# Optimization experiments

Hardware: AMD Instinct MI355X
Metric: run time of the kernel (lower is better)

## Reference

```python
import jax, jax.numpy as jnp
from jax import lax
import numpy as np

DEPTH, D_MODEL, D_INNER, D_STATE, DT_RANK = 24, 192, 384, 16, 12
EPS = 1e-5

def _layernorm(x, w, b):
    m = x.mean(-1, keepdims=True)
    v = ((x - m) ** 2).mean(-1, keepdims=True)
    return (x - m) * lax.rsqrt(v + EPS) * w + b

def _silu(x):
    return x * jax.nn.sigmoid(x)

def _mamba_mixer(x, in_w, cw, cb, xp_w, dtw, dtb, a_log, dvec, out_w):
    # x: (B, L, D_MODEL)
    B, L, _ = x.shape
    xz = jnp.einsum('bld,ed->ble', x, in_w)            # (B, L, 2*D_INNER)
    xi, z = xz[..., :D_INNER], xz[..., D_INNER:]
    # causal depthwise conv1d, kernel 4 (left-pad 3, truncate to L)
    xt = jnp.moveaxis(xi, 1, 2)                        # (B, D_INNER, L)
    xt = jnp.pad(xt, ((0, 0), (0, 0), (3, 0)))
    xt = lax.conv_general_dilated(xt, cw[:, None, :], (1,), 'VALID',
                                  dimension_numbers=('NCH', 'OIH', 'NCH'),
                                  feature_group_count=D_INNER)
    xt = _silu(xt + cb[None, :, None])
    xc = jnp.moveaxis(xt, 1, 2)                        # (B, L, D_INNER)
    x_dbl = jnp.einsum('bld,ed->ble', xc, xp_w)        # (B, L, DT_RANK+2*D_STATE)
    dt = x_dbl[..., :DT_RANK]
    Bm = x_dbl[..., DT_RANK:DT_RANK + D_STATE]         # (B, L, N)
    Cm = x_dbl[..., DT_RANK + D_STATE:]                # (B, L, N)
    delta = jax.nn.softplus(jnp.einsum('blr,dr->bld', dt, dtw) + dtb)  # (B, L, D_INNER)
    A = -jnp.exp(a_log)                                # (D_INNER, N)
    dA = jnp.exp(delta[..., None] * A)                 # (B, L, D_INNER, N)
    dBx = (delta * xc)[..., None] * Bm[:, :, None, :]  # (B, L, D_INNER, N)

    def step(h, inp):
        dA_t, dBx_t, C_t = inp
        h = dA_t * h + dBx_t
        y = jnp.einsum('bdn,bn->bd', h, C_t)
        return h, y

    h0 = jnp.zeros((B, D_INNER, D_STATE), x.dtype)
    _, ys = lax.scan(step, h0, (jnp.moveaxis(dA, 1, 0), jnp.moveaxis(dBx, 1, 0), jnp.moveaxis(Cm, 1, 0)))
    y = jnp.moveaxis(ys, 0, 1) + xc * dvec             # (B, L, D_INNER)
    y = y * _silu(z)
    return jnp.einsum('ble,de->bld', y, out_w)

def _forward(x, patch_w, patch_b, norm_w, norm_b, in_proj_w, conv_w, conv_b,
             x_proj_w, dt_w, dt_b, A_log, Dp, out_proj_w, normf_w, normf_b, head_w, head_b):
    # patch embed: conv 16x16 stride 16 -> (B, 192, 14, 14) -> (B, 196, 192)
    h = lax.conv_general_dilated(x, patch_w, (16, 16), 'VALID',
                                 dimension_numbers=('NCHW', 'OIHW', 'NCHW'))
    h = h + patch_b[None, :, None, None]
    B = h.shape[0]
    hidden = h.reshape(B, D_MODEL, -1).transpose(0, 2, 1)  # (B, L, D)
    residual = None
    for d in range(DEPTH):
        residual = hidden if residual is None else residual + hidden
        normed = _layernorm(residual, norm_w[d], norm_b[d])
        hidden = _mamba_mixer(normed, in_proj_w[d], conv_w[d], conv_b[d], x_proj_w[d],
                              dt_w[d], dt_b[d], A_log[d], Dp[d], out_proj_w[d])
    residual = residual + hidden
    feat = _layernorm(residual, normf_w, normf_b)
    pooled = feat.mean(axis=1)                           # final_pool_type='mean'
    return pooled @ head_w.T + head_b                    # (B, num_classes)

def setup_inputs() -> dict:
    key = jax.random.key(0)
    ks = jax.random.split(key, 16)
    s = 0.05
    return {
        'x': jax.random.normal(ks[0], (64, 3, 224, 224), jnp.float32),
        'patch_w': jax.random.normal(ks[1], (192, 3, 16, 16), jnp.float32) * s,
        'patch_b': jnp.zeros((192,), jnp.float32),
        'norm_w': jnp.ones((DEPTH, D_MODEL), jnp.float32),
        'norm_b': jnp.zeros((DEPTH, D_MODEL), jnp.float32),
        'in_proj_w': jax.random.normal(ks[2], (DEPTH, 2 * D_INNER, D_MODEL), jnp.float32) * s,
        'conv_w': jax.random.normal(ks[3], (DEPTH, D_INNER, 4), jnp.float32) * 0.3,
        'conv_b': jnp.zeros((DEPTH, D_INNER), jnp.float32),
        'x_proj_w': jax.random.normal(ks[4], (DEPTH, DT_RANK + 2 * D_STATE, D_INNER), jnp.float32) * s,
        'dt_w': jax.random.normal(ks[5], (DEPTH, D_INNER, DT_RANK), jnp.float32) * s,
        'dt_b': jax.random.uniform(ks[6], (DEPTH, D_INNER), jnp.float32, -4.0, -2.0),
        'A_log': jnp.log(jnp.broadcast_to(jnp.arange(1, D_STATE + 1, dtype=jnp.float32), (DEPTH, D_INNER, D_STATE))),
        'Dp': jnp.ones((DEPTH, D_INNER), jnp.float32),
        'out_proj_w': jax.random.normal(ks[7], (DEPTH, D_MODEL, D_INNER), jnp.float32) * s,
        'normf_w': jnp.ones((D_MODEL,), jnp.float32),
        'normf_b': jnp.zeros((D_MODEL,), jnp.float32),
        'head_w': jax.random.normal(ks[8], (1000, D_MODEL), jnp.float32) * s,
        'head_b': jnp.zeros((1000,), jnp.float32),
    }

def reference(x, patch_w, patch_b, norm_w, norm_b, in_proj_w, conv_w, conv_b,
              x_proj_w, dt_w, dt_b, A_log, Dp, out_proj_w, normf_w, normf_b, head_w, head_b):
    return _forward(x, patch_w, patch_b, norm_w, norm_b, in_proj_w, conv_w, conv_b,
                    x_proj_w, dt_w, dt_b, A_log, Dp, out_proj_w, normf_w, normf_b, head_w, head_b)
```

## Files before the change

kernel.cpp:

```cpp
#include <hip/hip_runtime.h>
#include <math.h>


#define DEPTH 24
#define DM 192
#define DI 384
#define DS 16
#define DR 12
#define SEQL 196
#define BATCH 64
#define MROWS (BATCH*SEQL)
#define XDP 8624
#define LOG2E 1.44269504088896340736f

typedef unsigned short ushort_t;
typedef __bf16 bf16x8 __attribute__((ext_vector_type(8)));
typedef float f32x4 __attribute__((ext_vector_type(4)));

__device__ __forceinline__ float sigmoidf_(float x) { return 1.f / (1.f + __expf(-x)); }

__device__ __forceinline__ ushort_t f2bf(float f) {
    union { float f; unsigned u; } c; c.f = f;
    unsigned u = c.u;
    return (ushort_t)((u + 0x7FFFu + ((u >> 16) & 1u)) >> 16);
}
__device__ __forceinline__ float bf2f(ushort_t u) {
    union { unsigned u; float f; } c; c.u = ((unsigned)u) << 16;
    return c.f;
}

__device__ __forceinline__ void load_lds16(const ushort_t* g, ushort_t* l) {
    __builtin_amdgcn_global_load_lds((__attribute__((address_space(1))) void*)g,
                                     (__attribute__((address_space(3))) void*)l, 16, 0, 0);
}

template<int CTRL>
__device__ __forceinline__ float dpp_mov(float oldv, float src) {
    return __builtin_bit_cast(float, __builtin_amdgcn_update_dpp(
        __builtin_bit_cast(int, oldv), __builtin_bit_cast(int, src),
        CTRL, 0xF, 0xF, false));
}

__device__ __forceinline__ float row16_sum(float v) {
    v += dpp_mov<0xB1>(0.f, v);
    v += dpp_mov<0x4E>(0.f, v);
    v += dpp_mov<0x141>(0.f, v);
    v += dpp_mov<0x140>(0.f, v);
    return v;
}

__global__ void f2bf4_kernel(const float* __restrict__ src, ushort_t* __restrict__ dst, int n4) {
    int i = blockIdx.x * 256 + threadIdx.x;
    if (i >= n4) return;
    float4 v = ((const float4*)src)[i];
    union { ushort_t s[4]; uint2 u; } o;
    o.s[0] = f2bf(v.x); o.s[1] = f2bf(v.y); o.s[2] = f2bf(v.z); o.s[3] = f2bf(v.w);
    ((uint2*)dst)[i] = o.u;
}

__global__ void xp_pad_kernel(const float* __restrict__ src, ushort_t* __restrict__ dst) {
    int i = blockIdx.x * 256 + threadIdx.x;
    if (i >= DEPTH * 64 * 384) return;
    int col = i % 384, row = (i / 384) & 63, d = i / (384 * 64);
    float v = (row < 44) ? src[(size_t)d * 44 * 384 + row * 384 + col] : 0.f;
    dst[i] = f2bf(v);
}

template<bool BF>
__global__ void ln_kernel(float* __restrict__ residual, const float* __restrict__ hidden,
                          const float* __restrict__ w, const float* __restrict__ b,
                          void* __restrict__ out_) {
    int wave = threadIdx.x >> 6, lane = threadIdx.x & 63;
    int row = blockIdx.x * 4 + wave;
    float* rr = residual + (size_t)row * DM;
    const float* hr = hidden + (size_t)row * DM;
    float v0 = rr[lane]       + hr[lane];
    float v1 = rr[lane + 64]  + hr[lane + 64];
    float v2 = rr[lane + 128] + hr[lane + 128];
    rr[lane] = v0; rr[lane + 64] = v1; rr[lane + 128] = v2;
    float s = v0 + v1 + v2;
    #pragma unroll
    for (int off = 32; off > 0; off >>= 1) s += __shfl_down(s, off);
    float mean = __shfl(s, 0) * (1.f / DM);
    float d0 = v0 - mean, d1 = v1 - mean, d2 = v2 - mean;
    float q = d0 * d0 + d1 * d1 + d2 * d2;
    #pragma unroll
    for (int off = 32; off > 0; off >>= 1) q += __shfl_down(q, off);
    float rstd = rsqrtf(__shfl(q, 0) * (1.f / DM) + 1e-5f);
    float o0 = d0 * rstd * w[lane]       + b[lane];
    float o1 = d1 * rstd * w[lane + 64]  + b[lane + 64];
    float o2 = d2 * rstd * w[lane + 128] + b[lane + 128];
    if constexpr (BF) {
        ushort_t* o = (ushort_t*)out_ + (size_t)row * DM;
        o[lane] = f2bf(o0); o[lane + 64] = f2bf(o1); o[lane + 128] = f2bf(o2);
    } else {
        float* o = (float*)out_ + (size_t)row * DM;
        o[lane] = o0; o[lane + 64] = o1; o[lane + 128] = o2;
    }
}

template<int BN, int WM, int WN, int NST, bool TC>
__global__ __launch_bounds__(256, 2) void gemm_mfma(const ushort_t* __restrict__ A,
        const ushort_t* __restrict__ W, float* __restrict__ C, int K, int ldC) {
    constexpr int FM = 128 / (WM * 16);
    constexpr int FN = BN / (WN * 16);
    __shared__ ushort_t sA[128 * 32];
    __shared__ ushort_t sB[BN * 32];
    const int t = threadIdx.x;
    const int wave = t >> 6, lane = t & 63;
    const int lr = lane & 15, lq = lane >> 4;
    const int wr = wave / WN, wc = wave % WN;
    const int m0 = blockIdx.x * 128, n0 = blockIdx.y * BN;
    const int wbase = t & ~63;

    f32x4 acc[FM][FN];
    #pragma unroll
    for (int i = 0; i < FM; i++)
        #pragma unroll
        for (int j = 0; j < FN; j++) acc[i][j] = f32x4{0.f, 0.f, 0.f, 0.f};

    for (int k0 = 0; k0 < K; k0 += 32) {
        __syncthreads();
        #pragma unroll
        for (int c = 0; c < 2; c++) {
            int s = c * 256 + t;
            int row = s >> 2;
            int quad = (s & 3) ^ ((row >> 1) & 3);
            load_lds16(A + (size_t)(m0 + row) * K + k0 + quad * 8,
                       sA + (size_t)(c * 256 + wbase) * 8);
        }
        #pragma unroll
        for (int c = 0; c < BN * 4 / 256; c++) {
            int s = c * 256 + t;
            int row = s >> 2;
            int quad = (s & 3) ^ ((row >> 1) & 3);
            load_lds16(W + (size_t)(n0 + row) * K + k0 + quad * 8,
                       sB + (size_t)(c * 256 + wbase) * 8);
        }
        __syncthreads();
        bf16x8 af[FM], bfr[FN];
        #pragma unroll
        for (int i = 0; i < FM; i++) {
            int row = wr * FM * 16 + i * 16 + lr;
            int slot = (row << 2) | (lq ^ ((row >> 1) & 3));
            af[i] = *(const bf16x8*)&sA[(size_t)slot * 8];
        }
        #pragma unroll
        for (int j = 0; j < FN; j++) {
            int row = wc * FN * 16 + j * 16 + lr;
            int slot = (row << 2) | (lq ^ ((row >> 1) & 3));
            bfr[j] = *(const bf16x8*)&sB[(size_t)slot * 8];
        }
        #pragma unroll
        for (int i = 0; i < FM; i++)
            #pragma unroll
            for (int j = 0; j < FN; j++)
                acc[i][j] = __builtin_amdgcn_mfma_f32_16x16x32_bf16(af[i], bfr[j], acc[i][j], 0, 0, 0);
    }
    int crow0 = m0 + wr * FM * 16 + lq * 4;
    int ccol0 = n0 + wc * FN * 16 + lr;
    if constexpr (TC) {
        #pragma unroll
        for (int i = 0; i < FM; i++) {
            int m = crow0 + i * 16;
            int bb = m / 196, l = m % 196;
            #pragma unroll
            for (int j = 0; j < FN; j++) {
                int col = ccol0 + j * 16;
                if (col < 44) {
                    float4 v = {acc[i][j][0], acc[i][j][1], acc[i][j][2], acc[i][j][3]};
                    *(float4*)(C + (size_t)bb * XDP + (size_t)col * 196 + l) = v;
                }
            }
        }
    } else {
        #pragma unroll
        for (int i = 0; i < FM; i++)
            #pragma unroll
            for (int j = 0; j < FN; j++) {
                if (wc * FN + j >= NST) continue;
                float* cp = C + (size_t)(crow0 + i * 16) * ldC + ccol0 + j * 16;
                #pragma unroll
                for (int r = 0; r < 4; r++) cp[(size_t)r * ldC] = acc[i][j][r];
            }
    }
}

__global__ __launch_bounds__(256, 2) void gemm_patch_mfma(const ushort_t* __restrict__ Xbf,
        const ushort_t* __restrict__ Wbf, const float* __restrict__ bias, float* __restrict__ C) {
    constexpr int FM = 2, FN = 4;
    __shared__ ushort_t sA[128 * 32];
    __shared__ ushort_t sB[64 * 32];
    const int t = threadIdx.x;
    const int wave = t >> 6, lane = t & 63;
    const int lr = lane & 15, lq = lane >> 4;
    const int m0 = blockIdx.x * 128, n0 = blockIdx.y * 64;
    const int wbase = t & ~63;

    const ushort_t* abase[2];
    int aquad[2];
    #pragma unroll
    for (int c = 0; c < 2; c++) {
        int s = c * 256 + t;
        int row = s >> 2;
        aquad[c] = (s & 3) ^ ((row >> 1) & 3);
        int m = m0 + row;
        int b = m / 196, r = m % 196, py = r / 14, px = r % 14;
        abase[c] = Xbf + (size_t)b * 150528 + py * 3584 + px * 16;
    }
    int brow = t >> 2;
    int bquad = (t & 3) ^ ((brow >> 1) & 3);
    const ushort_t* bbase = Wbf + (size_t)(n0 + brow) * 768 + bquad * 8;

    f32x4 acc[FM][FN];
    #pragma unroll
    for (int i = 0; i < FM; i++)
        #pragma unroll
        for (int j = 0; j < FN; j++) acc[i][j] = f32x4{0.f, 0.f, 0.f, 0.f};

    for (int k0 = 0; k0 < 768; k0 += 32) {
        __syncthreads();
        #pragma unroll
        for (int c = 0; c < 2; c++) {
            int k = k0 + aquad[c] * 8;
            int ci = k >> 8, ky = (k >> 4) & 15, kx0 = k & 15;
            load_lds16(abase[c] + ci * 50176 + ky * 224 + kx0,
                       sA + (size_t)(c * 256 + wbase) * 8);
        }
        load_lds16(bbase + k0, sB + (size_t)wbase * 8);
        __syncthreads();
        bf16x8 af[FM], bfr[FN];
        #pragma unroll
        for (int i = 0; i < FM; i++) {
            int row = wave * FM * 16 + i * 16 + lr;
            int slot = (row << 2) | (lq ^ ((row >> 1) & 3));
            af[i] = *(const bf16x8*)&sA[(size_t)slot * 8];
        }
        #pragma unroll
        for (int j = 0; j < FN; j++) {
            int row = j * 16 + lr;
            int slot = (row << 2) | (lq ^ ((row >> 1) & 3));
            bfr[j] = *(const bf16x8*)&sB[(size_t)slot * 8];
        }
        #pragma unroll
        for (int i = 0; i < FM; i++)
            #pragma unroll
            for (int j = 0; j < FN; j++)
                acc[i][j] = __builtin_amdgcn_mfma_f32_16x16x32_bf16(af[i], bfr[j], acc[i][j], 0, 0, 0);
    }
    int crow0 = m0 + wave * FM * 16 + lq * 4;
    int ccol0 = n0 + lr;
    #pragma unroll
    for (int i = 0; i < FM; i++)
        #pragma unroll
        for (int j = 0; j < FN; j++) {
            int col = ccol0 + j * 16;
            float bv = bias[col];
            float* cp = C + (size_t)(crow0 + i * 16) * DM + col;
            #pragma unroll
            for (int r = 0; r < 4; r++) cp[(size_t)r * DM] = acc[i][j][r] + bv;
        }
}

template<bool BIAS>
__global__ __launch_bounds__(256, 2) void gemm64(const float* __restrict__ A,
        const float* __restrict__ W, const float* __restrict__ bias,
        float* __restrict__ C, int M, int N, int K) {
    __shared__ float As[32][68];
    __shared__ float Ws[32][68];
    int t = threadIdx.x;
    int m0 = blockIdx.x * 64, n0 = blockIdx.y * 64;
    int lr = t >> 2, lk = (t & 3) * 4;
    int am = m0 + lr; bool avld = am < M;
    const float* Ap = A + (size_t)(avld ? am : 0) * K + lk;
    int wn = n0 + lr; bool wv = wn < N;
    const float* Wp = W + (size_t)(wv ? wn : 0) * K + lk;
    int tm = (t >> 4) * 4, tn = (t & 15) * 4;
    float acc[4][4];
    #pragma unroll
    for (int i = 0; i < 4; i++)
        #pragma unroll
        for (int j = 0; j < 4; j++) acc[i][j] = 0.f;

    for (int k0 = 0; k0 < K; k0 += 32) {
        float4 a0 = make_float4(0.f, 0.f, 0.f, 0.f), a1 = a0, w0 = a0, w1 = a0;
        if (avld) { a0 = *(const float4*)(Ap + k0); a1 = *(const float4*)(Ap + k0 + 16); }
        if (wv)   { w0 = *(const float4*)(Wp + k0); w1 = *(const float4*)(Wp + k0 + 16); }
        __syncthreads();
        As[lk + 0][lr] = a0.x; As[lk + 1][lr] = a0.y; As[lk + 2][lr] = a0.z; As[lk + 3][lr] = a0.w;
        As[lk + 16][lr] = a1.x; As[lk + 17][lr] = a1.y; As[lk + 18][lr] = a1.z; As[lk + 19][lr] = a1.w;
        Ws[lk + 0][lr] = w0.x; Ws[lk + 1][lr] = w0.y; Ws[lk + 2][lr] = w0.z; Ws[lk + 3][lr] = w0.w;
        Ws[lk + 16][lr] = w1.x; Ws[lk + 17][lr] = w1.y; Ws[lk + 18][lr] = w1.z; Ws[lk + 19][lr] = w1.w;
        __syncthreads();
        #pragma unroll
        for (int kk = 0; kk < 32; kk++) {
            float4 x0 = *(const float4*)&As[kk][tm];
            float4 y0 = *(const float4*)&Ws[kk][tn];
            float av[4] = {x0.x, x0.y, x0.z, x0.w};
            float bv[4] = {y0.x, y0.y, y0.z, y0.w};
            #pragma unroll
            for (int i = 0; i < 4; i++)
                #pragma unroll
                for (int j = 0; j < 4; j++) acc[i][j] = fmaf(av[i], bv[j], acc[i][j]);
        }
    }
    #pragma unroll
    for (int i = 0; i < 4; i++) {
        int m = m0 + tm + i;
        if (m >= M) continue;
        float* cr = C + (size_t)m * N;
        int n = n0 + tn;
        if (n < N) {
            float4 v = {acc[i][0], acc[i][1], acc[i][2], acc[i][3]};
            if (BIAS) { v.x += bias[n]; v.y += bias[n + 1]; v.z += bias[n + 2]; v.w += bias[n + 3]; }
            *(float4*)(cr + n) = v;
        }
    }
}

__global__ void conv_silu_kernel(const float* __restrict__ xz, const float* __restrict__ cw,
                                 const float* __restrict__ cb, ushort_t* __restrict__ xcbf) {
    int idx = blockIdx.x * 256 + threadIdx.x;
    if (idx >= MROWS * DI) return;
    int e = idx % DI; int bl = idx / DI; int l = bl % SEQL; int b = bl / SEQL;
    const float* base = xz + (size_t)(b * SEQL) * 768 + e;
    float w0 = cw[e * 4], w1 = cw[e * 4 + 1], w2 = cw[e * 4 + 2], w3 = cw[e * 4 + 3];
    float acc = cb[e];
    if (l >= 3) acc = fmaf(base[(size_t)(l - 3) * 768], w0, acc);
    if (l >= 2) acc = fmaf(base[(size_t)(l - 2) * 768], w1, acc);
    if (l >= 1) acc = fmaf(base[(size_t)(l - 1) * 768], w2, acc);
    acc = fmaf(base[(size_t)l * 768], w3, acc);
    xcbf[idx] = f2bf(acc * sigmoidf_(acc));
}

__global__ __launch_bounds__(512, 6) void scan_kernel(const float* __restrict__ xdt,
        const ushort_t* __restrict__ xcbf, const float* __restrict__ xz,
        const float* __restrict__ dtw, const float* __restrict__ dtb,
        const float* __restrict__ a_log, const float* __restrict__ Dp, ushort_t* __restrict__ y) {
    __shared__ float sd[44 * 196];
    __shared__ float dls[8][196];
    __shared__ float dus[8][196];
    __shared__ ushort_t xcs[8 * 200];
    __shared__ ushort_t ys[8 * 200];
    __shared__ float wdts[8][16];
    const int b = blockIdx.x, eg = blockIdx.y;
    const int tid = threadIdx.x;
    const int wave = tid >> 6, lane = tid & 63;
    const int e = eg * 8 + wave;
    const int n = lane & 15, c = lane >> 4;

    {
        const float4* src4 = (const float4*)(xdt + (size_t)b * XDP);
        float4* sd4 = (float4*)sd;
        for (int i = tid; i < XDP / 4; i += 512) sd4[i] = src4[i];
    }
    if (lane >= 16 && lane < 16 + DR) wdts[wave][lane - 16] = dtw[(size_t)e * DR + (lane - 16)];
    float4 zr0 = make_float4(0.f, 0.f, 0.f, 0.f), zr1 = zr0;
    if (tid < 196) {
        int l = tid;
        const ushort_t* xp = xcbf + (size_t)(b * SEQL + l) * DI + eg * 8;
        ushort4 xq0 = *(const ushort4*)xp;
        ushort4 xq1 = *(const ushort4*)(xp + 4);
        const float* zp = xz + (size_t)(b * SEQL + l) * 768 + DI + eg * 8;
        zr0 = *(const float4*)zp;
        zr1 = *(const float4*)(zp + 4);
        xcs[0 * 200 + l] = xq0.x; xcs[1 * 200 + l] = xq0.y;
        xcs[2 * 200 + l] = xq0.z; xcs[3 * 200 + l] = xq0.w;
        xcs[4 * 200 + l] = xq1.x; xcs[5 * 200 + l] = xq1.y;
        xcs[6 * 200 + l] = xq1.z; xcs[7 * 200 + l] = xq1.w;
    }
    __syncthreads();

    const float Avn = -__expf(a_log[(size_t)e * DS + n]) * LOG2E;
    const float db = dtb[e];

    if (lane < 49) {
        const int lb = lane * 4;
        f32x4 dt4 = {db, db, db, db};
        #pragma unroll
        for (int k = 0; k < DR; k++) {
            f32x4 r = *(const f32x4*)&sd[k * 196 + lb];
            dt4 += r * wdts[wave][k];
        }
        f32x4 d4;
        #pragma unroll
        for (int s = 0; s < 4; s++) {
            float v = dt4[s];
            d4[s] = (v > 20.f) ? v : __logf(1.f + __expf(v));
        }
        ushort4 xcq = *(const ushort4*)&xcs[wave * 200 + lb];
        f32x4 du4 = d4 * f32x4{bf2f(xcq.x), bf2f(xcq.y), bf2f(xcq.z), bf2f(xcq.w)};
        *(f32x4*)&dls[wave][lb] = d4;
        *(f32x4*)&dus[wave][lb] = du4;
    }

    const int t0 = (c == 0) ? 0 : 48 * c + 4;
    const int iters = (c == 0) ? 13 : 12;
    const float* Brow = &sd[(12 + n) * 196];
    const float* Crow = &sd[(28 + n) * 196];
    const float* dlw = dls[wave];
    const float* duw = dus[wave];

    float h = 0.f;
    f32x4 dsum = {0.f, 0.f, 0.f, 0.f};
    for (int i = 0; i < iters; i++) {
        int t = t0 + 4 * i;
        f32x4 dl = *(const f32x4*)&dlw[t];
        f32x4 du = *(const f32x4*)&duw[t];
        f32x4 Bn = *(const f32x4*)&Brow[t];
        dsum += dl;
        #pragma unroll
        for (int s = 0; s < 4; s++) {
            float dA = __builtin_amdgcn_exp2f(dl[s] * Avn);
            h = fmaf(h, dA, du[s] * Bn[s]);
        }
    }
    float P = __builtin_amdgcn_exp2f(Avn * (dsum[0] + dsum[1] + dsum[2] + dsum[3]));

    {
        float hp = __shfl_up(h, 16), pp = __shfl_up(P, 16);
        if (c >= 1) { h = fmaf(P, hp, h); P *= pp; }
        hp = __shfl_up(h, 32); pp = __shfl_up(P, 32);
        if (c >= 2) { h = fmaf(P, hp, h); P *= pp; }
    }
    float hin = __shfl_up(h, 16);
    if (c == 0) hin = 0.f;

    const float Dv = Dp[e];
    const ushort_t* xcw = &xcs[wave * 200];
    ushort_t* yw = &ys[wave * 200];
    h = hin;
    for (int i = 0; i < iters; i++) {
        int t = t0 + 4 * i;
        f32x4 dl = *(const f32x4*)&dlw[t];
        f32x4 du = *(const f32x4*)&duw[t];
        f32x4 Bn = *(const f32x4*)&Brow[t];
        f32x4 Cn = *(const f32x4*)&Crow[t];
        f32x4 yp;
        #pragma unroll
        for (int s = 0; s < 4; s++) {
            float dA = __builtin_amdgcn_exp2f(dl[s] * Avn);
            h = fmaf(h, dA, du[s] * Bn[s]);
            yp[s] = h * Cn[s];
        }
        #pragma unroll
        for (int s = 0; s < 4; s++) yp[s] = row16_sum(yp[s]);
        if (n < 4) {
            float ysel = (n == 0) ? yp[0] : (n == 1) ? yp[1] : (n == 2) ? yp[2] : yp[3];
            float xcsel = bf2f(xcw[t + n]);
            yw[t + n] = f2bf(fmaf(xcsel, Dv, ysel));
        }
    }
    __syncthreads();
    if (tid < 196) {
        int l = tid;
        float zv[8] = {zr0.x, zr0.y, zr0.z, zr0.w, zr1.x, zr1.y, zr1.z, zr1.w};
        union { ushort_t s[8]; ushort4 q[2]; } o;
        #pragma unroll
        for (int k = 0; k < 8; k++) {
            float yv = bf2f(ys[k * 200 + l]);
            float z = zv[k];
            o.s[k] = f2bf(yv * z * sigmoidf_(z));
        }
        ushort_t* yp = y + (size_t)(b * SEQL + l) * DI + eg * 8;
        *(ushort4*)yp = o.q[0];
        *(ushort4*)(yp + 4) = o.q[1];
    }
}

__global__ void pool_kernel(const float* __restrict__ normed, float* __restrict__ pooled) {
    int b = blockIdx.x, d = threadIdx.x;
    float s = 0.f;
    for (int l = 0; l < SEQL; l++) s += normed[(size_t)(b * SEQL + l) * DM + d];
    pooled[b * DM + d] = s * (1.f / 196.f);
}

extern "C" void kernel_launch(void* const* d_in, const int* in_sizes, int n_in,
                              void* d_out, int out_size, void* d_ws, size_t ws_size,
                              hipStream_t stream) {
    const float* x       = (const float*)d_in[0];
    const float* patch_w = (const float*)d_in[1];
    const float* patch_b = (const float*)d_in[2];
    const float* norm_w  = (const float*)d_in[3];
    const float* norm_b  = (const float*)d_in[4];
    const float* in_w    = (const float*)d_in[5];
    const float* conv_w  = (const float*)d_in[6];
    const float* conv_b  = (const float*)d_in[7];
    const float* xp_w    = (const float*)d_in[8];
    const float* dt_w    = (const float*)d_in[9];
    const float* dt_b    = (const float*)d_in[10];
    const float* A_log   = (const float*)d_in[11];
    const float* Dp      = (const float*)d_in[12];
    const float* out_w   = (const float*)d_in[13];
    const float* normf_w = (const float*)d_in[14];
    const float* normf_b = (const float*)d_in[15];
    const float* head_w  = (const float*)d_in[16];
    const float* head_b  = (const float*)d_in[17];

    float* ws = (float*)d_ws;
    float* residual     = ws;
    float* hidden       = ws + 2408448;
    float* xz           = ws + 4816896;
    ushort_t* xcbf      = (ushort_t*)(ws + 14450688);
    ushort_t* y_bf      = (ushort_t*)(ws + 16859136);
    ushort_t* x_bf      = (ushort_t*)(ws + 14450688);
    ushort_t* normed_bf = (ushort_t*)(ws + 19267584);
    float* xdbl_t       = ws + 20471808;
    float* pooled       = ws + 21023744;
    ushort_t* in_w_bf   = (ushort_t*)(ws + 21036032);
    ushort_t* out_w_bf  = (ushort_t*)(ws + 22805504);
    ushort_t* xp_w_bf   = (ushort_t*)(ws + 23690240);
    ushort_t* patch_w_bf= (ushort_t*)(ws + 23985152);

    (void)hipMemsetAsync(residual, 0, (size_t)2408448 * sizeof(float), stream);

    f2bf4_kernel<<<3456, 256, 0, stream>>>(in_w, in_w_bf, 884736);
    f2bf4_kernel<<<1728, 256, 0, stream>>>(out_w, out_w_bf, 442368);
    f2bf4_kernel<<<144, 256, 0, stream>>>(patch_w, patch_w_bf, 36864);
    f2bf4_kernel<<<9408, 256, 0, stream>>>(x, x_bf, 2408448);
    xp_pad_kernel<<<2304, 256, 0, stream>>>(xp_w, xp_w_bf);

    gemm_patch_mfma<<<dim3(98, 3), 256, 0, stream>>>(x_bf, patch_w_bf, patch_b, hidden);

    for (int d = 0; d < DEPTH; ++d) {
        ln_kernel<true><<<3136, 256, 0, stream>>>(residual, hidden, norm_w + d * DM,
                                                  norm_b + d * DM, normed_bf);
        gemm_mfma<192, 2, 2, 12, false><<<dim3(98, 4), 256, 0, stream>>>(normed_bf,
                in_w_bf + (size_t)d * 768 * 192, xz, 192, 768);
        conv_silu_kernel<<<18816, 256, 0, stream>>>(xz, conv_w + d * DI * 4, conv_b + d * DI, xcbf);
        gemm_mfma<64, 4, 1, 3, true><<<dim3(98, 1), 256, 0, stream>>>(xcbf,
                xp_w_bf + (size_t)d * 64 * 384, xdbl_t, 384, 196);
        scan_kernel<<<dim3(64, 48), 512, 0, stream>>>(xdbl_t, xcbf, xz, dt_w + d * DI * DR,
                dt_b + d * DI, A_log + d * DI * DS, Dp + d * DI, y_bf);
        gemm_mfma<64, 4, 1, 4, false><<<dim3(98, 3), 256, 0, stream>>>(y_bf,
                out_w_bf + (size_t)d * 192 * 384, hidden, 384, 192);
    }

    ln_kernel<false><<<3136, 256, 0, stream>>>(residual, hidden, normf_w, normf_b, xz);
    pool_kernel<<<64, 192, 0, stream>>>(xz, pooled);
    gemm64<true><<<dim3(1, 16), 256, 0, stream>>>(pooled, head_w, head_b, (float*)d_out, 64, 1000, 192);
}
```

Baseline: 3.165 ms.

## Shrink scan kernel LDS footprint by aliasing buffers to raise occupancy

The scan kernel's per-channel delta and delta*x buffers now reuse the dt-projection rows of the staged x_dbl tile after a barrier, and y is written back in place over the xc staging buffer. The dt weights are broadcast with lane shuffles instead of a shared array. Together these cut static shared memory from about 54KB to about 41KB per block, so more blocks can fit per CU, and launch bounds are raised to match. The cost is an extra barrier and a tighter register budget, which could cause spills.

```diff
diff --git a/kernel.cpp b/kernel.cpp
--- a/kernel.cpp
+++ b/kernel.cpp
@@ -333,16 +333,13 @@
     xcbf[idx] = f2bf(acc * sigmoidf_(acc));
 }
 
-__global__ __launch_bounds__(512, 6) void scan_kernel(const float* __restrict__ xdt,
+__global__ __launch_bounds__(512, 8) void scan_kernel(const float* __restrict__ xdt,
         const ushort_t* __restrict__ xcbf, const float* __restrict__ xz,
         const float* __restrict__ dtw, const float* __restrict__ dtb,
         const float* __restrict__ a_log, const float* __restrict__ Dp, ushort_t* __restrict__ y) {
     __shared__ float sd[44 * 196];
-    __shared__ float dls[8][196];
-    __shared__ float dus[8][196];
-    __shared__ ushort_t xcs[8 * 200];
-    __shared__ ushort_t ys[8 * 200];
-    __shared__ float wdts[8][16];
+    __shared__ float dux[4 * 196];
+    __shared__ ushort_t xcs[8 * 196];
     const int b = blockIdx.x, eg = blockIdx.y;
     const int tid = threadIdx.x;
     const int wave = tid >> 6, lane = tid & 63;
@@ -354,7 +351,8 @@
         float4* sd4 = (float4*)sd;
         for (int i = tid; i < XDP / 4; i += 512) sd4[i] = src4[i];
     }
-    if (lane >= 16 && lane < 16 + DR) wdts[wave][lane - 16] = dtw[(size_t)e * DR + (lane - 16)];
+    float wv = 0.f;
+    if (lane < DR) wv = dtw[(size_t)e * DR + lane];
     float4 zr0 = make_float4(0.f, 0.f, 0.f, 0.f), zr1 = zr0;
     if (tid < 196) {
         int l = tid;
@@ -364,42 +362,47 @@
         const float* zp = xz + (size_t)(b * SEQL + l) * 768 + DI + eg * 8;
         zr0 = *(const float4*)zp;
         zr1 = *(const float4*)(zp + 4);
-        xcs[0 * 200 + l] = xq0.x; xcs[1 * 200 + l] = xq0.y;
-        xcs[2 * 200 + l] = xq0.z; xcs[3 * 200 + l] = xq0.w;
-        xcs[4 * 200 + l] = xq1.x; xcs[5 * 200 + l] = xq1.y;
-        xcs[6 * 200 + l] = xq1.z; xcs[7 * 200 + l] = xq1.w;
+        xcs[0 * 196 + l] = xq0.x; xcs[1 * 196 + l] = xq0.y;
+        xcs[2 * 196 + l] = xq0.z; xcs[3 * 196 + l] = xq0.w;
+        xcs[4 * 196 + l] = xq1.x; xcs[5 * 196 + l] = xq1.y;
+        xcs[6 * 196 + l] = xq1.z; xcs[7 * 196 + l] = xq1.w;
     }
     __syncthreads();
 
     const float Avn = -__expf(a_log[(size_t)e * DS + n]) * LOG2E;
     const float db = dtb[e];
-
-    if (lane < 49) {
-        const int lb = lane * 4;
+    const bool act = lane < 49;
+    const int lb = act ? lane * 4 : 0;
+
+    f32x4 d4, du4;
+    {
         f32x4 dt4 = {db, db, db, db};
         #pragma unroll
         for (int k = 0; k < DR; k++) {
             f32x4 r = *(const f32x4*)&sd[k * 196 + lb];
-            dt4 += r * wdts[wave][k];
-        }
-        f32x4 d4;
+            dt4 += r * __shfl(wv, k);
+        }
         #pragma unroll
         for (int s = 0; s < 4; s++) {
             float v = dt4[s];
             d4[s] = (v > 20.f) ? v : __logf(1.f + __expf(v));
         }
-        ushort4 xcq = *(const ushort4*)&xcs[wave * 200 + lb];
-        f32x4 du4 = d4 * f32x4{bf2f(xcq.x), bf2f(xcq.y), bf2f(xcq.z), bf2f(xcq.w)};
-        *(f32x4*)&dls[wave][lb] = d4;
-        *(f32x4*)&dus[wave][lb] = du4;
+        ushort4 xcq = *(const ushort4*)&xcs[wave * 196 + lb];
+        du4 = d4 * f32x4{bf2f(xcq.x), bf2f(xcq.y), bf2f(xcq.z), bf2f(xcq.w)};
+    }
+    __syncthreads();
+    float* dlw = sd + wave * 196;
+    float* duw = (wave < 4) ? (sd + 8 * 196 + wave * 196)
+                            : (dux + (wave - 4) * 196);
+    if (act) {
+        *(f32x4*)&dlw[lb] = d4;
+        *(f32x4*)&duw[lb] = du4;
     }
 
     const int t0 = (c == 0) ? 0 : 48 * c + 4;
     const int iters = (c == 0) ? 13 : 12;
     const float* Brow = &sd[(12 + n) * 196];
     const float* Crow = &sd[(28 + n) * 196];
-    const float* dlw = dls[wave];
-    const float* duw = dus[wave];
 
     float h = 0.f;
     f32x4 dsum = {0.f, 0.f, 0.f, 0.f};
@@ -427,8 +430,7 @@
     if (c == 0) hin = 0.f;
 
     const float Dv = Dp[e];
-    const ushort_t* xcw = &xcs[wave * 200];
-    ushort_t* yw = &ys[wave * 200];
+    ushort_t* xcw = &xcs[wave * 196];
     h = hin;
     for (int i = 0; i < iters; i++) {
         int t = t0 + 4 * i;
@@ -448,7 +450,7 @@
         if (n < 4) {
             float ysel = (n == 0) ? yp[0] : (n == 1) ? yp[1] : (n == 2) ? yp[2] : yp[3];
             float xcsel = bf2f(xcw[t + n]);
-            yw[t + n] = f2bf(fmaf(xcsel, Dv, ysel));
+            xcw[t + n] = f2bf(fmaf(xcsel, Dv, ysel));
         }
     }
     __syncthreads();
@@ -458,7 +460,7 @@
         union { ushort_t s[8]; ushort4 q[2]; } o;
         #pragma unroll
         for (int k = 0; k < 8; k++) {
-            float yv = bf2f(ys[k * 200 + l]);
+            float yv = bf2f(xcs[k * 196 + l]);
             float z = zv[k];
             o.s[k] = f2bf(yv * z * sigmoidf_(z));
         }
```

Result: slower. 3.415 ms (+7.9%).
